# Kernel optimization log

Hardware: AMD Instinct MI355X
Metric: run time of the kernel (lower is better)

## Reference

```python
import jax, jax.numpy as jnp
import numpy as np

N_VIEWS, N_JOINTS, HM_H, HM_W = 5, 15, 128, 240
P = 4
VX = VY = VZ = 64
FX = FY = 253
FZ = 64
WHOLE_SIZE = np.array([8000.0, 8000.0, 2000.0], np.float32)
CENTER = np.array([0.0, -500.0, 800.0], np.float32)
IND_SIZE = np.array([2000.0, 2000.0, 2000.0], np.float32)
FINE = np.array([FX, FY, FZ], np.float32)


def setup_inputs() -> dict:
    key = jax.random.key(0)
    k1, k2, k3, k4 = jax.random.split(key, 4)
    heatmaps = jax.random.uniform(k1, (N_VIEWS, N_JOINTS, HM_H, HM_W), jnp.float32)
    # cached per-view fine-voxel sampling grid, clamped to [-1.1, 1.1] as in project_grid
    sample_grids = jax.random.uniform(k2, (N_VIEWS, FX, FY, FZ, 2), jnp.float32) * 2.2 - 1.1
    xyz = jnp.asarray(CENTER) + (jax.random.uniform(k3, (P, 3), jnp.float32) - 0.5) * jnp.asarray(WHOLE_SIZE - IND_SIZE)
    wh = jax.random.uniform(k4, (P, 2), jnp.float32, minval=0.2, maxval=1.0)
    proposal_centers = jnp.concatenate([xyz, jnp.zeros((P, 2), jnp.float32), wh], axis=1)
    return {"heatmaps": heatmaps, "sample_grids": sample_grids, "proposal_centers": proposal_centers}


def _grid_sample_2d(img, gx, gy):
    # img: [J,H,W]; gx,gy: [...]  bilinear, align_corners=True, zero padding (torch defaults)
    H, W = img.shape[-2:]
    px = (gx + 1.0) * 0.5 * (W - 1)
    py = (gy + 1.0) * 0.5 * (H - 1)
    x0 = jnp.floor(px)
    y0 = jnp.floor(py)
    wx1 = px - x0
    wy1 = py - y0

    def pick(xi, yi):
        ok = ((xi >= 0) & (xi < W) & (yi >= 0) & (yi < H)).astype(img.dtype)
        xc = jnp.clip(xi, 0, W - 1).astype(jnp.int32)
        yc = jnp.clip(yi, 0, H - 1).astype(jnp.int32)
        return img[:, yc, xc] * ok  # [J, ...]

    return (pick(x0, y0) * ((1 - wx1) * (1 - wy1))
            + pick(x0 + 1, y0) * (wx1 * (1 - wy1))
            + pick(x0, y0 + 1) * ((1 - wx1) * wy1)
            + pick(x0 + 1, y0 + 1) * (wx1 * wy1))


def _grids():
    # self.grids: computed once from INDIVIDUAL space size around whole-space center
    gx = np.linspace(-IND_SIZE[0] / 2, IND_SIZE[0] / 2, VX) + CENTER[0]
    gy = np.linspace(-IND_SIZE[1] / 2, IND_SIZE[1] / 2, VY) + CENTER[1]
    gz = np.linspace(-IND_SIZE[2] / 2, IND_SIZE[2] / 2, VZ) + CENTER[2]
    grid = np.stack(np.meshgrid(gx, gy, gz, indexing='ij'), axis=-1)  # [VX,VY,VZ,3]
    grids = np.stack([grid[:, :, 0, :2].reshape(-1, 2),
                      grid[:, 0, :, ::2].reshape(-1, 2),
                      grid[0, :, :, 1:].reshape(-1, 2)])
    return jnp.asarray(grids, jnp.float32)


def _forward(heatmaps, sample_grids, proposal_centers):
    pc = jax.lax.stop_gradient(proposal_centers)  # index math is non-differentiable
    mask_x = jnp.maximum(((1.0 - pc[:, 5]) / 2.0 * (VX - 1)).astype(jnp.int32), 0)
    mask_y = jnp.maximum(((1.0 - pc[:, 6]) / 2.0 * (VY - 1)).astype(jnp.int32), 0)
    ctl = jnp.round((pc[:, 0:3] + jnp.asarray(WHOLE_SIZE) / 2.0 - jnp.asarray(CENTER)
                     - jnp.asarray(IND_SIZE) / 2.0) / jnp.asarray(WHOLE_SIZE)
                    * (jnp.asarray(FINE) - 1.0)).astype(jnp.int32)
    x, y, z = ctl[:, 0], ctl[:, 1], ctl[:, 2]
    x_start = jnp.maximum(-x, 0) + mask_x
    x_end = jnp.minimum(FX - x, VX) - mask_x
    y_start = jnp.maximum(-y, 0) + mask_y
    y_end = jnp.minimum(FY - y, VY) - mask_y
    z_start = jnp.maximum(-z, 0)
    z_end = jnp.minimum(FZ - z, VZ)

    ix = jnp.arange(VX)
    iy = jnp.arange(VY)
    iz = jnp.arange(VZ)
    vx = (ix[None, :] >= x_start[:, None]) & (ix[None, :] < x_end[:, None])  # [P,VX]
    vy = (iy[None, :] >= y_start[:, None]) & (iy[None, :] < y_end[:, None])
    vz = (iz[None, :] >= z_start[:, None]) & (iz[None, :] < z_end[:, None])
    valid = vx[:, :, None, None] & vy[:, None, :, None] & vz[:, None, None, :]  # [P,VX,VY,VZ]

    # fine-grid indices for every output voxel (clipped; invalid ones masked out)
    fx = jnp.clip(x[:, None] + ix[None, :], 0, FX - 1)  # [P,VX]
    fy = jnp.clip(y[:, None] + iy[None, :], 0, FY - 1)
    fz = jnp.clip(z[:, None] + iz[None, :], 0, FZ - 1)
    sg = sample_grids[:, fx[:, :, None, None], fy[:, None, :, None], fz[:, None, None, :], :]  # [n,P,VX,VY,VZ,2]

    sampled = jax.vmap(_grid_sample_2d)(heatmaps, sg[..., 0], sg[..., 1])  # [n,J,P,VX,VY,VZ]
    cubes = jnp.mean(sampled, axis=0).transpose(1, 0, 2, 3, 4)  # [P,J,VX,VY,VZ]
    cubes = jnp.clip(cubes * valid[:, None, :, :, :].astype(cubes.dtype), 0.0, 1.0)
    return cubes


def reference(heatmaps, sample_grids, proposal_centers):
    cubes = _forward(heatmaps, sample_grids, proposal_centers)
    return (cubes, _grids())
```

## Files before the change

### kernel.cpp

```cpp
#include <hip/hip_runtime.h>

#define N_VIEWS 5
#define N_JOINTS 15
#define HM_H 128
#define HM_W 240
#define PB 4
#define VXn 64
#define VYn 64
#define VZn 64
#define FXn 253
#define FYn 253
#define FZn 64
#define JP 16

typedef float        vf2 __attribute__((ext_vector_type(2)));
typedef unsigned int vu4 __attribute__((ext_vector_type(4)));

__global__ void transpose_hm_kernel(const float* __restrict__ hm,
                                    unsigned char* __restrict__ T) {
    int t = blockIdx.x * blockDim.x + threadIdx.x;
    const int total = N_VIEWS * HM_H * HM_W;
    if (t >= total) return;
    int x = t % HM_W;
    int vy = t / HM_W;
    int y = vy % HM_H;
    int v = vy / HM_H;
    unsigned int w[4] = {0u, 0u, 0u, 0u};
#pragma unroll
    for (int j = 0; j < N_JOINTS; ++j) {
        float val = hm[(((size_t)v * N_JOINTS + j) * HM_H + y) * HM_W + x];
        float q = rintf(val * 255.0f);
        q = fminf(fmaxf(q, 0.0f), 255.0f);
        unsigned int b = (unsigned int)q;
        w[j >> 2] |= b << ((j & 3) * 8);
    }
    vu4* dst = (vu4*)(T + (size_t)t * JP);
    vu4 o; o.x = w[0]; o.y = w[1]; o.z = w[2]; o.w = w[3];
    *dst = o;
}

__global__ __launch_bounds__(256) void project_kernel(
    const unsigned char* __restrict__ hmT,
    const float* __restrict__ sg,
    const float* __restrict__ pc,
    float* __restrict__ out)
{
    const int iz = threadIdx.x;
    const int iy = blockIdx.x * 4 + threadIdx.y;
    const int ix = blockIdx.y;
    const int p  = blockIdx.z;

    const float pw = pc[p * 7 + 5];
    const float ph = pc[p * 7 + 6];
    int mask_x = max((int)((1.0f - pw) / 2.0f * (float)(VXn - 1)), 0);
    int mask_y = max((int)((1.0f - ph) / 2.0f * (float)(VYn - 1)), 0);

    float tx = pc[p * 7 + 0] + 4000.0f; tx = tx - 0.0f;      tx = tx - 1000.0f;
    float ty = pc[p * 7 + 1] + 4000.0f; ty = ty - (-500.0f); ty = ty - 1000.0f;
    float tz = pc[p * 7 + 2] + 1000.0f; tz = tz - 800.0f;    tz = tz - 1000.0f;
    tx = tx / 8000.0f * 252.0f;
    ty = ty / 8000.0f * 252.0f;
    tz = tz / 2000.0f * 63.0f;
    int cx = (int)rintf(tx);
    int cy = (int)rintf(ty);
    int cz = (int)rintf(tz);

    int x_start = max(-cx, 0) + mask_x;
    int x_end   = min(FXn - cx, VXn) - mask_x;
    int y_start = max(-cy, 0) + mask_y;
    int y_end   = min(FYn - cy, VYn) - mask_y;
    int z_start = max(-cz, 0);
    int z_end   = min(FZn - cz, VZn);

    const bool valid = (ix >= x_start && ix < x_end) &&
                       (iy >= y_start && iy < y_end) &&
                       (iz >= z_start && iz < z_end);

    const size_t out_base = ((((size_t)p * N_JOINTS) * VXn + ix) * VYn + iy) * VZn + iz;
    const size_t out_jstride = (size_t)VXn * VYn * VZn;

    unsigned long long mv = __ballot(valid ? 1 : 0);
    if (mv == 0ull) {
#pragma unroll
        for (int j = 0; j < N_JOINTS; ++j)
            __builtin_nontemporal_store(0.0f, &out[out_base + j * out_jstride]);
        return;
    }

    const int fx = min(max(cx + ix, 0), FXn - 1);
    const int fy = min(max(cy + iy, 0), FYn - 1);
    const int fz = min(max(cz + iz, 0), FZn - 1);

    const size_t sg_base = (((size_t)fx * FYn + fy) * FZn + fz) * 2;
    const size_t sg_vstride = (size_t)FXn * FYn * FZn * 2;

    vf2 g[N_VIEWS];
#pragma unroll
    for (int v = 0; v < N_VIEWS; ++v)
        g[v] = __builtin_nontemporal_load(
            (const vf2*)(sg + sg_base + (size_t)v * sg_vstride));

    float w00[N_VIEWS], w10[N_VIEWS], w01[N_VIEWS], w11[N_VIEWS];
    unsigned off00[N_VIEWS], off10[N_VIEWS], off01[N_VIEWS], off11[N_VIEWS];
#pragma unroll
    for (int v = 0; v < N_VIEWS; ++v) {
        float px = (g[v].x + 1.0f) * 0.5f * (float)(HM_W - 1);
        float py = (g[v].y + 1.0f) * 0.5f * (float)(HM_H - 1);
        float x0f = floorf(px), y0f = floorf(py);
        float wx1 = px - x0f,  wy1 = py - y0f;
        float wx0 = 1.0f - wx1, wy0 = 1.0f - wy1;
        float x1f = x0f + 1.0f, y1f = y0f + 1.0f;
        float okx0 = (x0f >= 0.0f && x0f < (float)HM_W) ? 1.0f : 0.0f;
        float okx1 = (x1f >= 0.0f && x1f < (float)HM_W) ? 1.0f : 0.0f;
        float oky0 = (y0f >= 0.0f && y0f < (float)HM_H) ? 1.0f : 0.0f;
        float oky1 = (y1f >= 0.0f && y1f < (float)HM_H) ? 1.0f : 0.0f;
        int x0 = min(max((int)x0f, 0), HM_W - 1);
        int x1 = min(max((int)x0f + 1, 0), HM_W - 1);
        int y0 = min(max((int)y0f, 0), HM_H - 1);
        int y1 = min(max((int)y0f + 1, 0), HM_H - 1);
        w00[v] = wx0 * wy0 * okx0 * oky0;
        w10[v] = wx1 * wy0 * okx1 * oky0;
        w01[v] = wx0 * wy1 * okx0 * oky1;
        w11[v] = wx1 * wy1 * okx1 * oky1;
        unsigned vbase = (unsigned)(v * HM_H * HM_W);
        off00[v] = (vbase + (unsigned)y0 * HM_W + (unsigned)x0) * JP;
        off10[v] = (vbase + (unsigned)y0 * HM_W + (unsigned)x1) * JP;
        off01[v] = (vbase + (unsigned)y1 * HM_W + (unsigned)x0) * JP;
        off11[v] = (vbase + (unsigned)y1 * HM_W + (unsigned)x1) * JP;
    }

    float acc[N_JOINTS];
#pragma unroll
    for (int j = 0; j < N_JOINTS; ++j) acc[j] = 0.0f;

#pragma unroll
    for (int b = 0; b < 2; ++b) {
        const int vbeg = (b == 0) ? 0 : 3;
        const int vend = (b == 0) ? 3 : N_VIEWS;
        vu4 tap[3][4];
#pragma unroll
        for (int v = vbeg; v < vend; ++v) {
            tap[v - vbeg][0] = *(const vu4*)(hmT + off00[v]);
            tap[v - vbeg][1] = *(const vu4*)(hmT + off10[v]);
            tap[v - vbeg][2] = *(const vu4*)(hmT + off01[v]);
            tap[v - vbeg][3] = *(const vu4*)(hmT + off11[v]);
        }
#pragma unroll
        for (int v = vbeg; v < vend; ++v) {
            const unsigned int* a = (const unsigned int*)&tap[v - vbeg][0];
            const unsigned int* bb = (const unsigned int*)&tap[v - vbeg][1];
            const unsigned int* c = (const unsigned int*)&tap[v - vbeg][2];
            const unsigned int* d = (const unsigned int*)&tap[v - vbeg][3];
#pragma unroll
            for (int j = 0; j < N_JOINTS; ++j) {
                int word = j >> 2, sh = (j & 3) * 8;
                float fa = (float)((a[word] >> sh) & 0xffu);
                float fb = (float)((bb[word] >> sh) & 0xffu);
                float fc = (float)((c[word] >> sh) & 0xffu);
                float fd = (float)((d[word] >> sh) & 0xffu);
                acc[j] += w00[v] * fa + w10[v] * fb + w01[v] * fc + w11[v] * fd;
            }
        }
    }

    const float scale = valid ? (0.2f / 255.0f) : 0.0f;
#pragma unroll
    for (int j = 0; j < N_JOINTS; ++j) {
        float vlu = acc[j] * scale;
        vlu = fminf(fmaxf(vlu, 0.0f), 1.0f);
        __builtin_nontemporal_store(vlu, &out[out_base + j * out_jstride]);
    }
}

__global__ void grids_kernel(float* __restrict__ out) {
    int t = blockIdx.x * blockDim.x + threadIdx.x;
    if (t >= 3 * 4096) return;
    int g = t / 4096;
    int idx = t % 4096;
    int a = idx / 64;
    int b = idx % 64;
    const float step = 2000.0f / 63.0f;
    float va = -1000.0f + (float)a * step;
    float vb = -1000.0f + (float)b * step;
    float o0, o1;
    if (g == 0)      { o0 = va + 0.0f;      o1 = vb + (-500.0f); }
    else if (g == 1) { o0 = va + 0.0f;      o1 = vb + 800.0f;    }
    else             { o0 = va + (-500.0f); o1 = vb + 800.0f;    }
    out[(size_t)t * 2 + 0] = o0;
    out[(size_t)t * 2 + 1] = o1;
}

extern "C" void kernel_launch(void* const* d_in, const int* in_sizes, int n_in,
                              void* d_out, int out_size, void* d_ws, size_t ws_size,
                              hipStream_t stream) {
    const float* hm = (const float*)d_in[0];
    const float* sg = (const float*)d_in[1];
    const float* pc = (const float*)d_in[2];
    float* out = (float*)d_out;

    unsigned char* T = (unsigned char*)d_ws;

    const int total = N_VIEWS * HM_H * HM_W;
    transpose_hm_kernel<<<(total + 255) / 256, 256, 0, stream>>>(hm, T);

    dim3 blk(64, 4, 1);
    dim3 grd(16, 64, 4);
    project_kernel<<<grd, blk, 0, stream>>>(T, sg, pc, out);

    const size_t grids_off = (size_t)PB * N_JOINTS * VXn * VYn * VZn;
    grids_kernel<<<(3 * 4096 + 255) / 256, 256, 0, stream>>>(out + grids_off);
}
```

Measured before the change: 64.19 us.

## Pack 2x2 bilinear neighborhoods into contiguous 64-byte records for gathers

```diff
diff --git a/kernel.cpp b/kernel.cpp
--- a/kernel.cpp
+++ b/kernel.cpp
@@ -31,16 +31,35 @@
         float val = hm[(((size_t)v * N_JOINTS + j) * HM_H + y) * HM_W + x];
         float q = rintf(val * 255.0f);
         q = fminf(fmaxf(q, 0.0f), 255.0f);
-        unsigned int b = (unsigned int)q;
-        w[j >> 2] |= b << ((j & 3) * 8);
+        w[j >> 2] |= ((unsigned int)q) << ((j & 3) * 8);
     }
     vu4* dst = (vu4*)(T + (size_t)t * JP);
     vu4 o; o.x = w[0]; o.y = w[1]; o.z = w[2]; o.w = w[3];
     *dst = o;
 }
 
+__global__ void pack2x2_kernel(const unsigned char* __restrict__ T1,
+                               unsigned char* __restrict__ T2) {
+    int t = blockIdx.x * blockDim.x + threadIdx.x;
+    const int total = N_VIEWS * HM_H * HM_W;
+    if (t >= total) return;
+    int x = t % HM_W;
+    int vy = t / HM_W;
+    int y = vy % HM_H;
+    int v = vy / HM_H;
+    int x1 = min(x + 1, HM_W - 1);
+    int y1 = min(y + 1, HM_H - 1);
+    const vu4* base = (const vu4*)T1;
+    vu4 r00 = base[((size_t)v * HM_H + y) * HM_W + x];
+    vu4 r01 = base[((size_t)v * HM_H + y) * HM_W + x1];
+    vu4 r10 = base[((size_t)v * HM_H + y1) * HM_W + x];
+    vu4 r11 = base[((size_t)v * HM_H + y1) * HM_W + x1];
+    vu4* dst = (vu4*)(T2 + (size_t)t * 64);
+    dst[0] = r00; dst[1] = r01; dst[2] = r10; dst[3] = r11;
+}
+
 __global__ __launch_bounds__(256) void project_kernel(
-    const unsigned char* __restrict__ hmT,
+    const unsigned char* __restrict__ T2,
     const float* __restrict__ sg,
     const float* __restrict__ pc,
     float* __restrict__ out)
@@ -100,8 +119,8 @@
         g[v] = __builtin_nontemporal_load(
             (const vf2*)(sg + sg_base + (size_t)v * sg_vstride));
 
-    float w00[N_VIEWS], w10[N_VIEWS], w01[N_VIEWS], w11[N_VIEWS];
-    unsigned off00[N_VIEWS], off10[N_VIEWS], off01[N_VIEWS], off11[N_VIEWS];
+    float W00[N_VIEWS], W01[N_VIEWS], W10[N_VIEWS], W11[N_VIEWS];
+    unsigned off[N_VIEWS];
 #pragma unroll
     for (int v = 0; v < N_VIEWS; ++v) {
         float px = (g[v].x + 1.0f) * 0.5f * (float)(HM_W - 1);
@@ -114,19 +133,22 @@
         float okx1 = (x1f >= 0.0f && x1f < (float)HM_W) ? 1.0f : 0.0f;
         float oky0 = (y0f >= 0.0f && y0f < (float)HM_H) ? 1.0f : 0.0f;
         float oky1 = (y1f >= 0.0f && y1f < (float)HM_H) ? 1.0f : 0.0f;
-        int x0 = min(max((int)x0f, 0), HM_W - 1);
-        int x1 = min(max((int)x0f + 1, 0), HM_W - 1);
-        int y0 = min(max((int)y0f, 0), HM_H - 1);
-        int y1 = min(max((int)y0f + 1, 0), HM_H - 1);
-        w00[v] = wx0 * wy0 * okx0 * oky0;
-        w10[v] = wx1 * wy0 * okx1 * oky0;
-        w01[v] = wx0 * wy1 * okx0 * oky1;
-        w11[v] = wx1 * wy1 * okx1 * oky1;
-        unsigned vbase = (unsigned)(v * HM_H * HM_W);
-        off00[v] = (vbase + (unsigned)y0 * HM_W + (unsigned)x0) * JP;
-        off10[v] = (vbase + (unsigned)y0 * HM_W + (unsigned)x1) * JP;
-        off01[v] = (vbase + (unsigned)y1 * HM_W + (unsigned)x0) * JP;
-        off11[v] = (vbase + (unsigned)y1 * HM_W + (unsigned)x1) * JP;
+        int x0i = (int)x0f, y0i = (int)y0f;
+        int rx = min(max(x0i, 0), HM_W - 1);
+        int ry = min(max(y0i, 0), HM_H - 1);
+        int ex = min(max(x0i + 1, 0), HM_W - 1) - rx;
+        int ey = min(max(y0i + 1, 0), HM_H - 1) - ry;
+        float w00 = wx0 * wy0 * okx0 * oky0;
+        float w10 = wx1 * wy0 * okx1 * oky0;
+        float w01 = wx0 * wy1 * okx0 * oky1;
+        float w11 = wx1 * wy1 * okx1 * oky1;
+        float fex = (float)ex, fey = (float)ey;
+        float gex = 1.0f - fex, gey = 1.0f - fey;
+        W00[v] = w00 + gex * w10 + gey * w01 + gex * gey * w11;
+        W01[v] = fex * (w10 + gey * w11);
+        W10[v] = fey * (w01 + gex * w11);
+        W11[v] = fex * fey * w11;
+        off[v] = ((unsigned)(v * HM_H + ry) * HM_W + (unsigned)rx) * 64u;
     }
 
     float acc[N_JOINTS];
@@ -137,20 +159,21 @@
     for (int b = 0; b < 2; ++b) {
         const int vbeg = (b == 0) ? 0 : 3;
         const int vend = (b == 0) ? 3 : N_VIEWS;
-        vu4 tap[3][4];
+        vu4 rec[3][4];
 #pragma unroll
         for (int v = vbeg; v < vend; ++v) {
-            tap[v - vbeg][0] = *(const vu4*)(hmT + off00[v]);
-            tap[v - vbeg][1] = *(const vu4*)(hmT + off10[v]);
-            tap[v - vbeg][2] = *(const vu4*)(hmT + off01[v]);
-            tap[v - vbeg][3] = *(const vu4*)(hmT + off11[v]);
+            const vu4* r = (const vu4*)(T2 + off[v]);
+            rec[v - vbeg][0] = r[0];
+            rec[v - vbeg][1] = r[1];
+            rec[v - vbeg][2] = r[2];
+            rec[v - vbeg][3] = r[3];
         }
 #pragma unroll
         for (int v = vbeg; v < vend; ++v) {
-            const unsigned int* a = (const unsigned int*)&tap[v - vbeg][0];
-            const unsigned int* bb = (const unsigned int*)&tap[v - vbeg][1];
-            const unsigned int* c = (const unsigned int*)&tap[v - vbeg][2];
-            const unsigned int* d = (const unsigned int*)&tap[v - vbeg][3];
+            const unsigned int* a = (const unsigned int*)&rec[v - vbeg][0];
+            const unsigned int* bb = (const unsigned int*)&rec[v - vbeg][1];
+            const unsigned int* c = (const unsigned int*)&rec[v - vbeg][2];
+            const unsigned int* d = (const unsigned int*)&rec[v - vbeg][3];
 #pragma unroll
             for (int j = 0; j < N_JOINTS; ++j) {
                 int word = j >> 2, sh = (j & 3) * 8;
@@ -158,7 +181,7 @@
                 float fb = (float)((bb[word] >> sh) & 0xffu);
                 float fc = (float)((c[word] >> sh) & 0xffu);
                 float fd = (float)((d[word] >> sh) & 0xffu);
-                acc[j] += w00[v] * fa + w10[v] * fb + w01[v] * fc + w11[v] * fd;
+                acc[j] += W00[v] * fa + W01[v] * fb + W10[v] * fc + W11[v] * fd;
             }
         }
     }
@@ -198,14 +221,16 @@
     const float* pc = (const float*)d_in[2];
     float* out = (float*)d_out;
 
-    unsigned char* T = (unsigned char*)d_ws;
-
     const int total = N_VIEWS * HM_H * HM_W;
-    transpose_hm_kernel<<<(total + 255) / 256, 256, 0, stream>>>(hm, T);
+    unsigned char* T1 = (unsigned char*)d_ws;
+    unsigned char* T2 = T1 + (size_t)total * JP;
+
+    transpose_hm_kernel<<<(total + 255) / 256, 256, 0, stream>>>(hm, T1);
+    pack2x2_kernel<<<(total + 255) / 256, 256, 0, stream>>>(T1, T2);
 
     dim3 blk(64, 4, 1);
     dim3 grd(16, 64, 4);
-    project_kernel<<<grd, blk, 0, stream>>>(T, sg, pc, out);
+    project_kernel<<<grd, blk, 0, stream>>>(T2, sg, pc, out);
 
     const size_t grids_off = (size_t)PB * N_JOINTS * VXn * VYn * VZn;
     grids_kernel<<<(3 * 4096 + 255) / 256, 256, 0, stream>>>(out + grids_off);
```

Result: slower. 73.14 us (+14.0%).

## Split views across threads with LDS reduction and fuse grid setup into prep

Applied to the files above, without the earlier changes.

```diff
diff --git a/kernel.cpp b/kernel.cpp
--- a/kernel.cpp
+++ b/kernel.cpp
@@ -16,37 +16,57 @@
 typedef float        vf2 __attribute__((ext_vector_type(2)));
 typedef unsigned int vu4 __attribute__((ext_vector_type(4)));
 
-__global__ void transpose_hm_kernel(const float* __restrict__ hm,
-                                    unsigned char* __restrict__ T) {
+#define T_TOTAL (N_VIEWS * HM_H * HM_W)
+#define G_TOTAL (3 * 4096)
+
+__global__ void prep_kernel(const float* __restrict__ hm,
+                            unsigned char* __restrict__ T,
+                            float* __restrict__ gout) {
     int t = blockIdx.x * blockDim.x + threadIdx.x;
-    const int total = N_VIEWS * HM_H * HM_W;
-    if (t >= total) return;
-    int x = t % HM_W;
-    int vy = t / HM_W;
-    int y = vy % HM_H;
-    int v = vy / HM_H;
-    unsigned int w[4] = {0u, 0u, 0u, 0u};
+    if (t < T_TOTAL) {
+        int x = t % HM_W;
+        int vy = t / HM_W;
+        int y = vy % HM_H;
+        int v = vy / HM_H;
+        unsigned int w[4] = {0u, 0u, 0u, 0u};
 #pragma unroll
-    for (int j = 0; j < N_JOINTS; ++j) {
-        float val = hm[(((size_t)v * N_JOINTS + j) * HM_H + y) * HM_W + x];
-        float q = rintf(val * 255.0f);
-        q = fminf(fmaxf(q, 0.0f), 255.0f);
-        unsigned int b = (unsigned int)q;
-        w[j >> 2] |= b << ((j & 3) * 8);
+        for (int j = 0; j < N_JOINTS; ++j) {
+            float val = hm[(((size_t)v * N_JOINTS + j) * HM_H + y) * HM_W + x];
+            float q = rintf(val * 255.0f);
+            q = fminf(fmaxf(q, 0.0f), 255.0f);
+            w[j >> 2] |= ((unsigned int)q) << ((j & 3) * 8);
+        }
+        vu4* dst = (vu4*)(T + (size_t)t * JP);
+        vu4 o; o.x = w[0]; o.y = w[1]; o.z = w[2]; o.w = w[3];
+        *dst = o;
+    } else {
+        int u = t - T_TOTAL;
+        if (u >= G_TOTAL) return;
+        int g = u / 4096;
+        int idx = u % 4096;
+        int a = idx / 64;
+        int b = idx % 64;
+        const float step = 2000.0f / 63.0f;
+        float va = -1000.0f + (float)a * step;
+        float vb = -1000.0f + (float)b * step;
+        float o0, o1;
+        if (g == 0)      { o0 = va + 0.0f;      o1 = vb + (-500.0f); }
+        else if (g == 1) { o0 = va + 0.0f;      o1 = vb + 800.0f;    }
+        else             { o0 = va + (-500.0f); o1 = vb + 800.0f;    }
+        gout[(size_t)u * 2 + 0] = o0;
+        gout[(size_t)u * 2 + 1] = o1;
     }
-    vu4* dst = (vu4*)(T + (size_t)t * JP);
-    vu4 o; o.x = w[0]; o.y = w[1]; o.z = w[2]; o.w = w[3];
-    *dst = o;
 }
 
-__global__ __launch_bounds__(256) void project_kernel(
+__global__ __launch_bounds__(320) void project_kernel(
     const unsigned char* __restrict__ hmT,
     const float* __restrict__ sg,
     const float* __restrict__ pc,
     float* __restrict__ out)
 {
     const int iz = threadIdx.x;
-    const int iy = blockIdx.x * 4 + threadIdx.y;
+    const int v  = threadIdx.y;
+    const int iy = blockIdx.x;
     const int ix = blockIdx.y;
     const int p  = blockIdx.z;
 
@@ -72,18 +92,19 @@
     int z_start = max(-cz, 0);
     int z_end   = min(FZn - cz, VZn);
 
-    const bool valid = (ix >= x_start && ix < x_end) &&
-                       (iy >= y_start && iy < y_end) &&
-                       (iz >= z_start && iz < z_end);
+    const bool row_valid = (ix >= x_start && ix < x_end) &&
+                           (iy >= y_start && iy < y_end);
 
-    const size_t out_base = ((((size_t)p * N_JOINTS) * VXn + ix) * VYn + iy) * VZn + iz;
+    const size_t out_base = ((((size_t)p * N_JOINTS) * VXn + ix) * VYn + iy) * VZn;
     const size_t out_jstride = (size_t)VXn * VYn * VZn;
 
-    unsigned long long mv = __ballot(valid ? 1 : 0);
-    if (mv == 0ull) {
+    if (!row_valid) {
 #pragma unroll
-        for (int j = 0; j < N_JOINTS; ++j)
-            __builtin_nontemporal_store(0.0f, &out[out_base + j * out_jstride]);
+        for (int k = 0; k < 3; ++k) {
+            int idx = v * 64 + iz + k * 320;
+            int j = idx >> 6, z = idx & 63;
+            __builtin_nontemporal_store(0.0f, &out[out_base + j * out_jstride + z]);
+        }
         return;
     }
 
@@ -91,103 +112,71 @@
     const int fy = min(max(cy + iy, 0), FYn - 1);
     const int fz = min(max(cz + iz, 0), FZn - 1);
 
-    const size_t sg_base = (((size_t)fx * FYn + fy) * FZn + fz) * 2;
-    const size_t sg_vstride = (size_t)FXn * FYn * FZn * 2;
+    const vf2 g = __builtin_nontemporal_load(
+        (const vf2*)(sg + ((((size_t)v * FXn + fx) * FYn + fy) * FZn + fz) * 2));
 
-    vf2 g[N_VIEWS];
+    float px = (g.x + 1.0f) * 0.5f * (float)(HM_W - 1);
+    float py = (g.y + 1.0f) * 0.5f * (float)(HM_H - 1);
+    float x0f = floorf(px), y0f = floorf(py);
+    float wx1 = px - x0f,  wy1 = py - y0f;
+    float wx0 = 1.0f - wx1, wy0 = 1.0f - wy1;
+    float x1f = x0f + 1.0f, y1f = y0f + 1.0f;
+    float okx0 = (x0f >= 0.0f && x0f < (float)HM_W) ? 1.0f : 0.0f;
+    float okx1 = (x1f >= 0.0f && x1f < (float)HM_W) ? 1.0f : 0.0f;
+    float oky0 = (y0f >= 0.0f && y0f < (float)HM_H) ? 1.0f : 0.0f;
+    float oky1 = (y1f >= 0.0f && y1f < (float)HM_H) ? 1.0f : 0.0f;
+    int x0 = min(max((int)x0f, 0), HM_W - 1);
+    int x1 = min(max((int)x0f + 1, 0), HM_W - 1);
+    int y0 = min(max((int)y0f, 0), HM_H - 1);
+    int y1 = min(max((int)y0f + 1, 0), HM_H - 1);
+    float w00 = wx0 * wy0 * okx0 * oky0;
+    float w10 = wx1 * wy0 * okx1 * oky0;
+    float w01 = wx0 * wy1 * okx0 * oky1;
+    float w11 = wx1 * wy1 * okx0 * oky1;
+    w11 = wx1 * wy1 * okx1 * oky1;
+
+    const unsigned vb = (unsigned)(v * HM_H);
+    unsigned off00 = ((vb + (unsigned)y0) * HM_W + (unsigned)x0) * JP;
+    unsigned off10 = ((vb + (unsigned)y0) * HM_W + (unsigned)x1) * JP;
+    unsigned off01 = ((vb + (unsigned)y1) * HM_W + (unsigned)x0) * JP;
+    unsigned off11 = ((vb + (unsigned)y1) * HM_W + (unsigned)x1) * JP;
+
+    vu4 ta = __builtin_nontemporal_load((const vu4*)(hmT + off00));
+    vu4 tb = __builtin_nontemporal_load((const vu4*)(hmT + off10));
+    vu4 tc = __builtin_nontemporal_load((const vu4*)(hmT + off01));
+    vu4 td = __builtin_nontemporal_load((const vu4*)(hmT + off11));
+
+    __shared__ float part[5 * 64 * 17];
+    const int lbase = (v * 64 + iz) * 17;
+    const unsigned int* a = (const unsigned int*)&ta;
+    const unsigned int* b = (const unsigned int*)&tb;
+    const unsigned int* c = (const unsigned int*)&tc;
+    const unsigned int* d = (const unsigned int*)&td;
 #pragma unroll
-    for (int v = 0; v < N_VIEWS; ++v)
-        g[v] = __builtin_nontemporal_load(
-            (const vf2*)(sg + sg_base + (size_t)v * sg_vstride));
-
-    float w00[N_VIEWS], w10[N_VIEWS], w01[N_VIEWS], w11[N_VIEWS];
-    unsigned off00[N_VIEWS], off10[N_VIEWS], off01[N_VIEWS], off11[N_VIEWS];
-#pragma unroll
-    for (int v = 0; v < N_VIEWS; ++v) {
-        float px = (g[v].x + 1.0f) * 0.5f * (float)(HM_W - 1);
-        float py = (g[v].y + 1.0f) * 0.5f * (float)(HM_H - 1);
-        float x0f = floorf(px), y0f = floorf(py);
-        float wx1 = px - x0f,  wy1 = py - y0f;
-        float wx0 = 1.0f - wx1, wy0 = 1.0f - wy1;
-        float x1f = x0f + 1.0f, y1f = y0f + 1.0f;
-        float okx0 = (x0f >= 0.0f && x0f < (float)HM_W) ? 1.0f : 0.0f;
-        float okx1 = (x1f >= 0.0f && x1f < (float)HM_W) ? 1.0f : 0.0f;
-        float oky0 = (y0f >= 0.0f && y0f < (float)HM_H) ? 1.0f : 0.0f;
-        float oky1 = (y1f >= 0.0f && y1f < (float)HM_H) ? 1.0f : 0.0f;
-        int x0 = min(max((int)x0f, 0), HM_W - 1);
-        int x1 = min(max((int)x0f + 1, 0), HM_W - 1);
-        int y0 = min(max((int)y0f, 0), HM_H - 1);
-        int y1 = min(max((int)y0f + 1, 0), HM_H - 1);
-        w00[v] = wx0 * wy0 * okx0 * oky0;
-        w10[v] = wx1 * wy0 * okx1 * oky0;
-        w01[v] = wx0 * wy1 * okx0 * oky1;
-        w11[v] = wx1 * wy1 * okx1 * oky1;
-        unsigned vbase = (unsigned)(v * HM_H * HM_W);
-        off00[v] = (vbase + (unsigned)y0 * HM_W + (unsigned)x0) * JP;
-        off10[v] = (vbase + (unsigned)y0 * HM_W + (unsigned)x1) * JP;
-        off01[v] = (vbase + (unsigned)y1 * HM_W + (unsigned)x0) * JP;
-        off11[v] = (vbase + (unsigned)y1 * HM_W + (unsigned)x1) * JP;
+    for (int j = 0; j < N_JOINTS; ++j) {
+        int word = j >> 2, sh = (j & 3) * 8;
+        float fa = (float)((a[word] >> sh) & 0xffu);
+        float fb = (float)((b[word] >> sh) & 0xffu);
+        float fc = (float)((c[word] >> sh) & 0xffu);
+        float fd = (float)((d[word] >> sh) & 0xffu);
+        part[lbase + j] = w00 * fa + w10 * fb + w01 * fc + w11 * fd;
     }
-
-    float acc[N_JOINTS];
-#pragma unroll
-    for (int j = 0; j < N_JOINTS; ++j) acc[j] = 0.0f;
+    __syncthreads();
 
 #pragma unroll
-    for (int b = 0; b < 2; ++b) {
-        const int vbeg = (b == 0) ? 0 : 3;
-        const int vend = (b == 0) ? 3 : N_VIEWS;
-        vu4 tap[3][4];
-#pragma unroll
-        for (int v = vbeg; v < vend; ++v) {
-            tap[v - vbeg][0] = *(const vu4*)(hmT + off00[v]);
-            tap[v - vbeg][1] = *(const vu4*)(hmT + off10[v]);
-            tap[v - vbeg][2] = *(const vu4*)(hmT + off01[v]);
-            tap[v - vbeg][3] = *(const vu4*)(hmT + off11[v]);
-        }
-#pragma unroll
-        for (int v = vbeg; v < vend; ++v) {
-            const unsigned int* a = (const unsigned int*)&tap[v - vbeg][0];
-            const unsigned int* bb = (const unsigned int*)&tap[v - vbeg][1];
-            const unsigned int* c = (const unsigned int*)&tap[v - vbeg][2];
-            const unsigned int* d = (const unsigned int*)&tap[v - vbeg][3];
-#pragma unroll
-            for (int j = 0; j < N_JOINTS; ++j) {
-                int word = j >> 2, sh = (j & 3) * 8;
-                float fa = (float)((a[word] >> sh) & 0xffu);
-                float fb = (float)((bb[word] >> sh) & 0xffu);
-                float fc = (float)((c[word] >> sh) & 0xffu);
-                float fd = (float)((d[word] >> sh) & 0xffu);
-                acc[j] += w00[v] * fa + w10[v] * fb + w01[v] * fc + w11[v] * fd;
-            }
-        }
+    for (int k = 0; k < 3; ++k) {
+        int idx = v * 64 + iz + k * 320;
+        int j = idx >> 6, z = idx & 63;
+        float s = part[(0 * 64 + z) * 17 + j]
+                + part[(1 * 64 + z) * 17 + j]
+                + part[(2 * 64 + z) * 17 + j]
+                + part[(3 * 64 + z) * 17 + j]
+                + part[(4 * 64 + z) * 17 + j];
+        bool zok = (z >= z_start) && (z < z_end);
+        float vlu = zok ? s * (0.2f / 255.0f) : 0.0f;
+        vlu = fminf(fmaxf(vlu, 0.0f), 1.0f);
+        __builtin_nontemporal_store(vlu, &out[out_base + j * out_jstride + z]);
     }
-
-    const float scale = valid ? (0.2f / 255.0f) : 0.0f;
-#pragma unroll
-    for (int j = 0; j < N_JOINTS; ++j) {
-        float vlu = acc[j] * scale;
-        vlu = fminf(fmaxf(vlu, 0.0f), 1.0f);
-        __builtin_nontemporal_store(vlu, &out[out_base + j * out_jstride]);
-    }
-}
-
-__global__ void grids_kernel(float* __restrict__ out) {
-    int t = blockIdx.x * blockDim.x + threadIdx.x;
-    if (t >= 3 * 4096) return;
-    int g = t / 4096;
-    int idx = t % 4096;
-    int a = idx / 64;
-    int b = idx % 64;
-    const float step = 2000.0f / 63.0f;
-    float va = -1000.0f + (float)a * step;
-    float vb = -1000.0f + (float)b * step;
-    float o0, o1;
-    if (g == 0)      { o0 = va + 0.0f;      o1 = vb + (-500.0f); }
-    else if (g == 1) { o0 = va + 0.0f;      o1 = vb + 800.0f;    }
-    else             { o0 = va + (-500.0f); o1 = vb + 800.0f;    }
-    out[(size_t)t * 2 + 0] = o0;
-    out[(size_t)t * 2 + 1] = o1;
 }
 
 extern "C" void kernel_launch(void* const* d_in, const int* in_sizes, int n_in,
@@ -200,13 +189,11 @@
 
     unsigned char* T = (unsigned char*)d_ws;
 
-    const int total = N_VIEWS * HM_H * HM_W;
-    transpose_hm_kernel<<<(total + 255) / 256, 256, 0, stream>>>(hm, T);
+    const size_t grids_off = (size_t)PB * N_JOINTS * VXn * VYn * VZn;
+    const int prep_total = T_TOTAL + G_TOTAL;
+    prep_kernel<<<(prep_total + 255) / 256, 256, 0, stream>>>(hm, T, out + grids_off);
 
-    dim3 blk(64, 4, 1);
-    dim3 grd(16, 64, 4);
+    dim3 blk(64, 5, 1);
+    dim3 grd(64, 64, 4);
     project_kernel<<<grd, blk, 0, stream>>>(T, sg, pc, out);
-
-    const size_t grids_off = (size_t)PB * N_JOINTS * VXn * VYn * VZn;
-    grids_kernel<<<(3 * 4096 + 255) / 256, 256, 0, stream>>>(out + grids_off);
 }
```

Measured after the change: 104.1 us. 62.1% more time.
